# Kernel tuning notes

Hardware: AMD Instinct MI355X
Metric: run time of the kernel (lower is better)

The kernel has to match this reference:

```python
import jax, jax.numpy as jnp
import numpy as np

B, N, D2H, U = 16, 1024, 1024, 512  # batch of sentences, tokens, 2*lstm_dims, hidden_units


def setup_inputs() -> dict:
    key = jax.random.key(0)
    ks = jax.random.split(key, 7)
    s = 1.0 / np.sqrt(D2H)
    return {
        "x": jax.random.normal(ks[0], (B, N, D2H), dtype=jnp.float32),
        "W_h": jax.random.normal(ks[1], (U, D2H), dtype=jnp.float32) * s,
        "b_h": jax.random.normal(ks[2], (U,), dtype=jnp.float32) * 0.01,
        "W_m": jax.random.normal(ks[3], (U, D2H), dtype=jnp.float32) * s,
        "b_m": jax.random.normal(ks[4], (U,), dtype=jnp.float32) * 0.01,
        "w_out": jax.random.normal(ks[5], (U,), dtype=jnp.float32) * (1.0 / np.sqrt(U)),
        "b_out": jax.random.normal(ks[6], (), dtype=jnp.float32) * 0.01,
    }


def reference(x, W_h, b_h, W_m, b_m, w_out, b_out):
    # headfov[i] = W_h @ x_i + b_h ; modfov[j] = W_m @ x_j + b_m
    H = jnp.einsum("bnd,ud->bnu", x, W_h) + b_h  # [B, N, U]
    M = jnp.einsum("bnd,ud->bnu", x, W_m) + b_m  # [B, N, U]
    # score[i,j] = w_out . (H_i + M_j) + b_out  (outLayer is linear, so it
    # distributes over the add; avoids materializing an [B,N,N,U] tensor)
    sH = jnp.einsum("bnu,u->bn", H, w_out)  # [B, N]
    sM = jnp.einsum("bnu,u->bn", M, w_out)  # [B, N]
    scores = sH[:, :, None] + sM[:, None, :] + b_out  # [B, N, N]
    return scores
```

## Files before the change

### kernel.cpp

```cpp
#include <hip/hip_runtime.h>

#define BB 16
#define NN 1024
#define DD 1024
#define UU 512

__global__ __launch_bounds__(256) void prep_kernel(
    const float* __restrict__ W_h, const float* __restrict__ W_m,
    const float* __restrict__ b_h, const float* __restrict__ b_m,
    const float* __restrict__ w_out, const float* __restrict__ b_out,
    float* __restrict__ v_h, float* __restrict__ v_m, float* __restrict__ Cc) {
    int t = threadIdx.x;
    int blk = blockIdx.x;
    if (blk < 128) {
        const float* W = (blk < 64) ? W_h : W_m;
        float* v = (blk < 64) ? v_h : v_m;
        int b = blk & 63;
        int d = (b & 3) * 256 + t;
        int u0 = (b >> 2) * 32;
        float acc = 0.f;
        #pragma unroll
        for (int k = 0; k < 32; ++k) {
            acc += W[(size_t)(u0 + k) * DD + d] * w_out[u0 + k];
        }
        atomicAdd(v + d, acc);
    } else {
        __shared__ float red[256];
        float acc = 0.f;
        for (int u = t; u < UU; u += 256) acc += (b_h[u] + b_m[u]) * w_out[u];
        red[t] = acc;
        __syncthreads();
        for (int s = 128; s > 0; s >>= 1) {
            if (t < s) red[t] += red[t + s];
            __syncthreads();
        }
        if (t == 0) *Cc = red[0] + b_out[0];
    }
}

__global__ __launch_bounds__(256) void row_dots_kernel(
    const float* __restrict__ x,
    const float* __restrict__ v_h, const float* __restrict__ v_m,
    const float* __restrict__ Cc,
    float* __restrict__ sH, float* __restrict__ sM) {
    int t = threadIdx.x;
    int wave = t >> 6, lane = t & 63;
    int row = blockIdx.x * 4 + wave;
    const float4* xr = (const float4*)(x + (size_t)row * DD);
    const float4* vh = (const float4*)v_h;
    const float4* vm = (const float4*)v_m;

    float ah = 0.f, am = 0.f;
    #pragma unroll
    for (int k = 0; k < 4; ++k) {
        int idx = lane + 64 * k;
        float4 xv = xr[idx];
        float4 hv = vh[idx];
        float4 mv = vm[idx];
        ah += xv.x * hv.x + xv.y * hv.y + xv.z * hv.z + xv.w * hv.w;
        am += xv.x * mv.x + xv.y * mv.y + xv.z * mv.z + xv.w * mv.w;
    }
    #pragma unroll
    for (int off = 32; off > 0; off >>= 1) {
        ah += __shfl_down(ah, off, 64);
        am += __shfl_down(am, off, 64);
    }
    if (lane == 0) {
        sH[row] = ah + *Cc;
        sM[row] = am;
    }
}

__global__ __launch_bounds__(256) void scores_kernel(
    const float* __restrict__ sH, const float* __restrict__ sM,
    float4* __restrict__ out) {
    int bi = blockIdx.x;
    int j4 = threadIdx.x;
    float h = sH[bi];
    const float4* mrow = (const float4*)(sM + (bi & ~(NN - 1)));
    float4 m = mrow[j4];
    float4 o;
    o.x = h + m.x;
    o.y = h + m.y;
    o.z = h + m.z;
    o.w = h + m.w;
    out[(size_t)bi * (NN / 4) + j4] = o;
}

extern "C" void kernel_launch(void* const* d_in, const int* in_sizes, int n_in,
                              void* d_out, int out_size, void* d_ws, size_t ws_size,
                              hipStream_t stream) {
    const float* x     = (const float*)d_in[0];
    const float* W_h   = (const float*)d_in[1];
    const float* b_h   = (const float*)d_in[2];
    const float* W_m   = (const float*)d_in[3];
    const float* b_m   = (const float*)d_in[4];
    const float* w_out = (const float*)d_in[5];
    const float* b_out = (const float*)d_in[6];
    float* out = (float*)d_out;

    float* ws  = (float*)d_ws;
    float* v_h = ws;
    float* v_m = ws + 1024;
    float* Cc  = ws + 2048;
    float* sH  = ws + 4096;
    float* sM  = ws + 4096 + 16384;

    (void)hipMemsetAsync(ws, 0, 2048 * sizeof(float), stream);

    prep_kernel<<<129, 256, 0, stream>>>(W_h, W_m, b_h, b_m, w_out, b_out, v_h, v_m, Cc);
    row_dots_kernel<<<BB * NN / 4, 256, 0, stream>>>(x, v_h, v_m, Cc, sH, sM);
    scores_kernel<<<BB * NN, 256, 0, stream>>>(sH, sM, (float4*)out);
}
```

Baseline: 127.2 us.

## Replace atomic reduction with partial sums and stage vectors in LDS

The prep kernel now writes 8 per-chunk partial projection vectors instead of atomically accumulating into zeroed buffers, which removes the memset launch and the atomics. The row-dot kernel sums those partials into shared memory once per block, then each wave handles 4 rows, cutting the block count by 4x. The cost is redundant partial summation in every block (16 KB of reads per block) and fewer blocks to hide latency.

After: 139.7 us. +9.9%, slower.

```diff
diff --git a/kernel.cpp b/kernel.cpp
--- a/kernel.cpp
+++ b/kernel.cpp
@@ -9,21 +9,23 @@
     const float* __restrict__ W_h, const float* __restrict__ W_m,
     const float* __restrict__ b_h, const float* __restrict__ b_m,
     const float* __restrict__ w_out, const float* __restrict__ b_out,
-    float* __restrict__ v_h, float* __restrict__ v_m, float* __restrict__ Cc) {
+    float* __restrict__ pH, float* __restrict__ pM, float* __restrict__ Cc) {
     int t = threadIdx.x;
     int blk = blockIdx.x;
-    if (blk < 128) {
-        const float* W = (blk < 64) ? W_h : W_m;
-        float* v = (blk < 64) ? v_h : v_m;
-        int b = blk & 63;
-        int d = (b & 3) * 256 + t;
-        int u0 = (b >> 2) * 32;
+    if (blk < 64) {
+        int m = blk >> 5;
+        int r = blk & 31;
+        int d = (r & 3) * 256 + t;
+        int c = r >> 2;
+        int u0 = c * 64;
+        const float* W = m ? W_m : W_h;
+        float* P = (m ? pM : pH) + (size_t)c * DD;
         float acc = 0.f;
         #pragma unroll
-        for (int k = 0; k < 32; ++k) {
+        for (int k = 0; k < 64; ++k) {
             acc += W[(size_t)(u0 + k) * DD + d] * w_out[u0 + k];
         }
-        atomicAdd(v + d, acc);
+        P[d] = acc;
     } else {
         __shared__ float red[256];
         float acc = 0.f;
@@ -40,34 +42,55 @@
 
 __global__ __launch_bounds__(256) void row_dots_kernel(
     const float* __restrict__ x,
-    const float* __restrict__ v_h, const float* __restrict__ v_m,
+    const float* __restrict__ pH, const float* __restrict__ pM,
     const float* __restrict__ Cc,
     float* __restrict__ sH, float* __restrict__ sM) {
+    __shared__ float lvh[DD];
+    __shared__ float lvm[DD];
     int t = threadIdx.x;
+    #pragma unroll
+    for (int j = 0; j < 4; ++j) {
+        int d = t + j * 256;
+        float sh = 0.f, sm = 0.f;
+        #pragma unroll
+        for (int c = 0; c < 8; ++c) {
+            sh += pH[(size_t)c * DD + d];
+            sm += pM[(size_t)c * DD + d];
+        }
+        lvh[d] = sh;
+        lvm[d] = sm;
+    }
+    __syncthreads();
+
+    float C = *Cc;
     int wave = t >> 6, lane = t & 63;
-    int row = blockIdx.x * 4 + wave;
-    const float4* xr = (const float4*)(x + (size_t)row * DD);
-    const float4* vh = (const float4*)v_h;
-    const float4* vm = (const float4*)v_m;
+    int rbase = blockIdx.x * 16 + wave * 4;
+    const float4* vh = (const float4*)lvh;
+    const float4* vm = (const float4*)lvm;
 
-    float ah = 0.f, am = 0.f;
     #pragma unroll
-    for (int k = 0; k < 4; ++k) {
-        int idx = lane + 64 * k;
-        float4 xv = xr[idx];
-        float4 hv = vh[idx];
-        float4 mv = vm[idx];
-        ah += xv.x * hv.x + xv.y * hv.y + xv.z * hv.z + xv.w * hv.w;
-        am += xv.x * mv.x + xv.y * mv.y + xv.z * mv.z + xv.w * mv.w;
-    }
-    #pragma unroll
-    for (int off = 32; off > 0; off >>= 1) {
-        ah += __shfl_down(ah, off, 64);
-        am += __shfl_down(am, off, 64);
-    }
-    if (lane == 0) {
-        sH[row] = ah + *Cc;
-        sM[row] = am;
+    for (int r = 0; r < 4; ++r) {
+        int row = rbase + r;
+        const float4* xr = (const float4*)(x + (size_t)row * DD);
+        float ah = 0.f, am = 0.f;
+        #pragma unroll
+        for (int k = 0; k < 4; ++k) {
+            int idx = lane + 64 * k;
+            float4 xv = xr[idx];
+            float4 hv = vh[idx];
+            float4 mv = vm[idx];
+            ah += xv.x * hv.x + xv.y * hv.y + xv.z * hv.z + xv.w * hv.w;
+            am += xv.x * mv.x + xv.y * mv.y + xv.z * mv.z + xv.w * mv.w;
+        }
+        #pragma unroll
+        for (int off = 32; off > 0; off >>= 1) {
+            ah += __shfl_down(ah, off, 64);
+            am += __shfl_down(am, off, 64);
+        }
+        if (lane == 0) {
+            sH[row] = ah + C;
+            sM[row] = am;
+        }
     }
 }
 
@@ -99,16 +122,15 @@
     const float* b_out = (const float*)d_in[6];
     float* out = (float*)d_out;
 
-    float* ws  = (float*)d_ws;
-    float* v_h = ws;
-    float* v_m = ws + 1024;
-    float* Cc  = ws + 2048;
-    float* sH  = ws + 4096;
-    float* sM  = ws + 4096 + 16384;
+    float* ws = (float*)d_ws;
+    float* pH = ws;
+    float* pM = ws + 8192;
+    float* Cc = ws + 16384;
+    float* sH = ws + 16640;
+    float* sM = ws + 16640 + 16384;
 
-    (void)hipMemsetAsync(ws, 0, 2048 * sizeof(float), stream);
 
-    prep_kernel<<<129, 256, 0, stream>>>(W_h, W_m, b_h, b_m, w_out, b_out, v_h, v_m, Cc);
-    row_dots_kernel<<<BB * NN / 4, 256, 0, stream>>>(x, v_h, v_m, Cc, sH, sM);
+    prep_kernel<<<65, 256, 0, stream>>>(W_h, W_m, b_h, b_m, w_out, b_out, pH, pM, Cc);
+    row_dots_kernel<<<BB * NN / 16, 256, 0, stream>>>(x, pH, pM, Cc, sH, sM);
     scores_kernel<<<BB * NN, 256, 0, stream>>>(sH, sM, (float4*)out);
 }
```
